# Performance work log

Measured on AMD Instinct MI355X. Metric: run time of the kernel, lower is better.

## Reference

```python
import jax, jax.numpy as jnp
import numpy as np

N = 50000
E = 1600000
IN_DIM = 256
HID = 64
OUT = 16
NEG_SLOPE = 0.01


def setup_inputs() -> dict:
    key = jax.random.key(0)
    ks = jax.random.split(key, 6)
    local_features = jax.random.normal(ks[0], (N, IN_DIM), dtype=jnp.float32)
    edge_index = jax.random.randint(ks[1], (2, E), 0, N, dtype=jnp.int32)
    W0 = jax.random.normal(ks[2], (IN_DIM, HID), dtype=jnp.float32) * 0.05
    a0 = jax.random.normal(ks[3], (2 * HID, 1), dtype=jnp.float32) * 0.05
    W1 = jax.random.normal(ks[4], (HID, OUT), dtype=jnp.float32) * 0.05
    a1 = jax.random.normal(ks[5], (2 * OUT, 1), dtype=jnp.float32) * 0.05
    return {"local_features": local_features, "edge_index": edge_index,
            "W0": W0, "a0": a0, "W1": W1, "a1": a1}


def _segment_softmax(scores, seg, num_segments):
    # softmax over edges sharing the same row (destination) id
    smax = jax.ops.segment_max(scores, seg, num_segments=num_segments)
    ex = jnp.exp(scores - smax[seg])
    ssum = jax.ops.segment_sum(ex, seg, num_segments=num_segments)
    return ex / ssum[seg]


def _gat_layer(H, row, col, W, a, apply_elu):
    d = W.shape[1]
    Hw = H @ W                                   # [N, d]
    # score_e = leaky_relu([Hw[row] || Hw[col]] @ a) = leaky_relu(pr[row] + pc[col])
    pr = Hw @ a[:d, 0]                           # [N]
    pc = Hw @ a[d:, 0]                           # [N]
    s = pr[row] + pc[col]                        # [E]
    s = jnp.where(s >= 0, s, NEG_SLOPE * s)      # leaky_relu
    att = _segment_softmax(s, row, Hw.shape[0])  # per-row sparse softmax (dim=1)
    # out[row] = sum_e att_e * Hw[col_e]
    out = jax.ops.segment_sum(att[:, None] * Hw[col], row, num_segments=Hw.shape[0])
    if apply_elu:
        out = jnp.where(out > 0, out, jnp.expm1(out))  # elu
    return out


def reference(local_features, edge_index, W0, a0, W1, a1):
    row = edge_index[0]
    col = edge_index[1]
    H = _gat_layer(local_features, row, col, W0, a0, apply_elu=True)
    H = _gat_layer(H, row, col, W1, a1, apply_elu=False)
    return jax.nn.log_softmax(H, axis=1)
```

## Files before the change

kernel.cpp:

```cpp
#include <hip/hip_runtime.h>
#include <hip/hip_bf16.h>
#include <math.h>

#define NN 50000
#define NE 1600000
#define BSH 9
#define BCK 98
#define BCAP 20480
#define GEMM_BLKS 98

typedef __attribute__((ext_vector_type(8))) short bf16x8;
typedef __attribute__((ext_vector_type(4))) float f32x4;
typedef __attribute__((ext_vector_type(2))) float f32x2;

__device__ __forceinline__ short f2bf(float f) {
    return (short)((__float_as_uint(f) + 0x8000u) >> 16);
}
__device__ __forceinline__ float lo16(unsigned u) { return __uint_as_float(u << 16); }
__device__ __forceinline__ float hi16(unsigned u) { return __uint_as_float(u & 0xffff0000u); }
__device__ __forceinline__ unsigned enc_f(float f) {
    unsigned u = __float_as_uint(f);
    return (u & 0x80000000u) ? ~u : (u | 0x80000000u);
}
__device__ __forceinline__ float dec_f(unsigned e) {
    return (e & 0x80000000u) ? __uint_as_float(e & 0x7FFFFFFFu)
                             : __uint_as_float(~e);
}

__global__ void setup_kernel(int* __restrict__ gcursor, unsigned* __restrict__ maxes,
                             unsigned* __restrict__ max1s,
                             const float* __restrict__ W, ushort* __restrict__ WTg) {
    int b = blockIdx.x;
    int t = threadIdx.x;
    if (b == 0) {
        if (t < BCK) gcursor[t] = t * BCAP;
        if (t < 2) maxes[t] = 0u;
        for (int i = t; i < 512; i += 256) max1s[i] = 0u;
    } else {
        int i = (b - 1) * 256 + t;
        int n = i >> 8, k = i & 255;
        WTg[n * 264 + k] = (ushort)f2bf(W[k * 64 + n]);
    }
}

__global__ void __launch_bounds__(1024) gbinA_kernel(
        const float* __restrict__ X,
        const ushort* __restrict__ WTg,
        const float* __restrict__ a,
        __hip_bfloat16* __restrict__ Hwb,
        float* __restrict__ pr,
        float* __restrict__ pc,
        unsigned* __restrict__ max0,
        const int* __restrict__ row, const int* __restrict__ col,
        int* __restrict__ gcursor, unsigned* __restrict__ staging) {
    __shared__ union SH {
        struct {
            unsigned lds_stage[8192];
            unsigned lds_addr[8192];
            int lds_cnt[128];
            int lds_off[128];
            int wg_goff[128];
            int wtot[2];
        } a;
        struct {
            ushort Wt[64 * 264];
            unsigned bmax;
        } g;
    } sh;
    int tid = threadIdx.x;

    if (blockIdx.x < GEMM_BLKS) {
        if (tid == 0) sh.g.bmax = 0u;
        {
            const uint* src = (const uint*)WTg;
            uint* dst = (uint*)sh.g.Wt;
            for (int i = tid; i < 64 * 132; i += 1024) dst[i] = src[i];
        }
        __syncthreads();
        int g256 = tid >> 8, t256 = tid & 255;
        int lane = t256 & 63, wid = t256 >> 6;
        int c = lane & 15, quad = lane >> 4;
        const ushort* wtp[4];
#pragma unroll
        for (int g = 0; g < 4; ++g) wtp[g] = &sh.g.Wt[(g * 16 + c) * 264 + quad * 8];
        float aA[4], aB[4];
#pragma unroll
        for (int g = 0; g < 4; ++g) { aA[g] = a[g * 16 + c]; aB[g] = a[64 + g * 16 + c]; }

        int row0 = blockIdx.x * 512 + g256 * 128 + wid * 16;
        float qmax = -1e30f;

#pragma unroll
        for (int tt = 0; tt < 2; ++tt) {
            int rt = row0 + tt * 64;
            int arow = rt + c; if (arow >= NN) arow = NN - 1;
            const float* xbase = X + (size_t)arow * 256 + quad * 8;
            f32x4 acc[4];
#pragma unroll
            for (int g = 0; g < 4; ++g) acc[g] = (f32x4){0.f, 0.f, 0.f, 0.f};

#pragma unroll
            for (int k0 = 0; k0 < 256; k0 += 32) {
                float4 xa = *(const float4*)(xbase + k0);
                float4 xb = *(const float4*)(xbase + k0 + 4);
                bf16x8 af;
                af[0] = f2bf(xa.x); af[1] = f2bf(xa.y); af[2] = f2bf(xa.z); af[3] = f2bf(xa.w);
                af[4] = f2bf(xb.x); af[5] = f2bf(xb.y); af[6] = f2bf(xb.z); af[7] = f2bf(xb.w);
#pragma unroll
                for (int g = 0; g < 4; ++g) {
                    bf16x8 bg = *(const bf16x8*)(wtp[g] + k0);
                    acc[g] = __builtin_amdgcn_mfma_f32_16x16x32_bf16(af, bg, acc[g], 0, 0, 0);
                }
            }

#pragma unroll
            for (int r = 0; r < 4; ++r) {
                int rr = rt + quad * 4 + r;
                float v0 = acc[0][r], v1 = acc[1][r], v2 = acc[2][r], v3 = acc[3][r];
                if (rr < NN) {
                    __hip_bfloat16* hp = Hwb + (size_t)rr * 64 + c;
                    hp[0]  = __float2bfloat16(v0);
                    hp[16] = __float2bfloat16(v1);
                    hp[32] = __float2bfloat16(v2);
                    hp[48] = __float2bfloat16(v3);
                }
                float pv = v0 * aA[0] + v1 * aA[1] + v2 * aA[2] + v3 * aA[3];
                float qv = v0 * aB[0] + v1 * aB[1] + v2 * aB[2] + v3 * aB[3];
#pragma unroll
                for (int off = 8; off; off >>= 1) {
                    pv += __shfl_xor(pv, off);
                    qv += __shfl_xor(qv, off);
                }
                if (c == 0 && rr < NN) { pr[rr] = pv; pc[rr] = qv; }
                if (rr < NN) qmax = fmaxf(qmax, qv);
            }
        }
        qmax = fmaxf(qmax, __shfl_xor(qmax, 16));
        qmax = fmaxf(qmax, __shfl_xor(qmax, 32));
        if (lane == 0) atomicMax(&sh.g.bmax, enc_f(qmax));
        __syncthreads();
        if (tid == 0) atomicMax(max0, sh.g.bmax);
        return;
    }

    int t = tid;
    int lane = t & 63;
    int w = t >> 6;
    int nbin = gridDim.x - GEMM_BLKS;

    for (int cb = (blockIdx.x - GEMM_BLKS) * 8192; cb < NE; cb += nbin * 8192) {
        int cnt_edges = NE - cb; if (cnt_edges > 8192) cnt_edges = 8192;
        if (t < 128) sh.a.lds_cnt[t] = 0;
        __syncthreads();
        int myb[8]; int mylo[8]; unsigned mypk[8];
        int e0 = cb + t * 8;
        if (t * 8 + 7 < cnt_edges) {
            int4 r0 = *(const int4*)(row + e0);
            int4 r1 = *(const int4*)(row + e0 + 4);
            int4 c0 = *(const int4*)(col + e0);
            int4 c1 = *(const int4*)(col + e0 + 4);
            int rr[8] = {r0.x, r0.y, r0.z, r0.w, r1.x, r1.y, r1.z, r1.w};
            int cc[8] = {c0.x, c0.y, c0.z, c0.w, c1.x, c1.y, c1.z, c1.w};
            #pragma unroll
            for (int i = 0; i < 8; ++i) {
                int b = rr[i] >> BSH;
                myb[i] = b;
                mypk[i] = ((unsigned)(rr[i] & 511) << 16) | (unsigned)cc[i];
                mylo[i] = atomicAdd(&sh.a.lds_cnt[b], 1);
            }
        } else {
            #pragma unroll
            for (int i = 0; i < 8; ++i) {
                int idx = t * 8 + i;
                myb[i] = -1;
                if (idx < cnt_edges) {
                    int e = cb + idx;
                    int r = row[e], c = col[e];
                    myb[i] = r >> BSH;
                    mypk[i] = ((unsigned)(r & 511) << 16) | (unsigned)c;
                    mylo[i] = atomicAdd(&sh.a.lds_cnt[myb[i]], 1);
                }
            }
        }
        __syncthreads();
        int v = (t < 128) ? sh.a.lds_cnt[t] : 0;
        int x = v;
        #pragma unroll
        for (int off = 1; off < 64; off <<= 1) {
            int y = __shfl_up(x, off);
            if (lane >= off) x += y;
        }
        if (t < 128 && lane == 63) sh.a.wtot[w] = x;
        __syncthreads();
        int add = (w == 1) ? sh.a.wtot[0] : 0;
        if (t < 128) sh.a.lds_off[t] = x - v + add;
        if (t < BCK) {
            int cc2 = sh.a.lds_cnt[t];
            sh.a.wg_goff[t] = cc2 ? atomicAdd(&gcursor[t], cc2) : 0;
        }
        __syncthreads();
        #pragma unroll
        for (int i = 0; i < 8; ++i) if (myb[i] >= 0) {
            int p = sh.a.lds_off[myb[i]] + mylo[i];
            sh.a.lds_stage[p] = mypk[i];
            sh.a.lds_addr[p] = (unsigned)(sh.a.wg_goff[myb[i]] + mylo[i]);
        }
        __syncthreads();
        for (int i = t; i < cnt_edges; i += 1024)
            staging[sh.a.lds_addr[i]] = sh.a.lds_stage[i];
        __syncthreads();
    }
}

__global__ void __launch_bounds__(1024) binB_kernel(
        const int* __restrict__ gcursor,
        const unsigned* __restrict__ staging,
        int* __restrict__ rowptr,
        ushort* __restrict__ colperm) {
    __shared__ int bsc[128];
    __shared__ int bw[2];
    __shared__ int cur[512];
    __shared__ int wls8[8];
    __shared__ ushort lds_col[BCAP];
    int b = blockIdx.x;
    int t = threadIdx.x;
    int lane = t & 63;
    int w = t >> 6;

    if (t < 128) {
        int v = 0;
        if (t < BCK) {
            v = gcursor[t] - t * BCAP;
            if (v > BCAP) v = BCAP;
        }
        int x = v;
        #pragma unroll
        for (int off = 1; off < 64; off <<= 1) {
            int y = __shfl_up(x, off);
            if (lane >= off) x += y;
        }
        if (lane == 63) bw[w] = x;
        bsc[t] = x - v;
    }
    __syncthreads();
    int gbase = bsc[b] + ((b >= 64) ? bw[0] : 0);
    int cnt = gcursor[b] - b * BCAP;
    if (cnt > BCAP) cnt = BCAP;
    if (b == 0 && t == 0) rowptr[NN] = bw[0] + bw[1];
    int rbase = b << BSH;
    int nrows = NN - rbase; if (nrows > 512) nrows = 512;
    const unsigned* sb = staging + (size_t)b * BCAP;

    unsigned ev[20];
    #pragma unroll
    for (int j = 0; j < 5; ++j) {
        int i0 = t * 4 + j * 4096;
        uint4 val = {0u, 0u, 0u, 0u};
        if (i0 + 3 < cnt) {
            val = *(const uint4*)(sb + i0);
        } else {
            if (i0 + 0 < cnt) val.x = sb[i0 + 0];
            if (i0 + 1 < cnt) val.y = sb[i0 + 1];
            if (i0 + 2 < cnt) val.z = sb[i0 + 2];
            if (i0 + 3 < cnt) val.w = sb[i0 + 3];
        }
        ev[j * 4 + 0] = val.x; ev[j * 4 + 1] = val.y;
        ev[j * 4 + 2] = val.z; ev[j * 4 + 3] = val.w;
    }

    if (t < 512) cur[t] = 0;
    __syncthreads();
    #pragma unroll
    for (int j = 0; j < 5; ++j) {
        #pragma unroll
        for (int l = 0; l < 4; ++l) {
            int idx = t * 4 + j * 4096 + l;
            if (idx < cnt) atomicAdd(&cur[ev[j * 4 + l] >> 16], 1);
        }
    }
    __syncthreads();
    int v = 0, x = 0;
    if (t < 512) {
        v = cur[t];
        x = v;
        #pragma unroll
        for (int off = 1; off < 64; off <<= 1) {
            int y = __shfl_up(x, off);
            if (lane >= off) x += y;
        }
        if (lane == 63) wls8[w] = x;
    }
    __syncthreads();
    if (t < 8) {
        int s = wls8[t];
        #pragma unroll
        for (int off = 1; off < 8; off <<= 1) {
            int y = __shfl_up(s, off, 8);
            if ((t & 7) >= off) s += y;
        }
        wls8[t] = s;
    }
    __syncthreads();
    int excl = 0;
    if (t < 512) {
        excl = x - v + ((w > 0) ? wls8[w - 1] : 0);
        if (t < nrows) rowptr[rbase + t] = gbase + excl;
    }
    __syncthreads();
    if (t < 512) cur[t] = excl;
    __syncthreads();
    #pragma unroll
    for (int j = 0; j < 5; ++j) {
        #pragma unroll
        for (int l = 0; l < 4; ++l) {
            int idx = t * 4 + j * 4096 + l;
            if (idx < cnt) {
                unsigned e = ev[j * 4 + l];
                int pos = atomicAdd(&cur[e >> 16], 1);
                lds_col[pos] = (ushort)(e & 0xFFFFu);
            }
        }
    }
    __syncthreads();
    for (int i = t; i < cnt; i += 1024)
        colperm[gbase + i] = lds_col[i];
}

__global__ void __launch_bounds__(256) node0_kernel(
        const int* __restrict__ rowptr,
        const ushort* __restrict__ colperm,
        const float* __restrict__ pr,
        const float* __restrict__ pc,
        const unsigned* __restrict__ pcmax,
        const ushort* __restrict__ Hwb,
        const float* __restrict__ W1,
        const float* __restrict__ a1,
        __hip_bfloat16* __restrict__ Hw1b,
        float* __restrict__ pr1,
        float* __restrict__ pc1,
        unsigned* __restrict__ max1s) {
    __shared__ float W1s[64 * 17];
    __shared__ float a1s[32];
    __shared__ float hbuf[4][64];
    __shared__ unsigned long long wcbuf[4][64];
    __shared__ unsigned bmax1;
    int t = threadIdx.x;
    if (t == 0) bmax1 = 0u;
    for (int i = t; i < 64 * 16; i += 256)
        W1s[(i >> 4) * 17 + (i & 15)] = W1[i];
    if (t < 32) a1s[t] = a1[t];
    __syncthreads();

    int lane = t & 63;
    int wid = t >> 6;
    int node = blockIdx.x * 4 + wid;
    int k = lane & 15, q = lane >> 4;
    int start = rowptr[node], end = rowptr[node + 1];
    float pri = pr[node];
    float m = pri + dec_f(*pcmax);
    m = (m >= 0.f) ? m : 0.01f * m;

    float wsum = 0.f;
    f32x2 accA = {0.f, 0.f}, accB = {0.f, 0.f};
    for (int base = start; base < end; base += 64) {
        int n = end - base; if (n > 64) n = 64;
        float wv = 0.f; unsigned cv = 0;
        if (lane < n) {
            cv = (unsigned)colperm[base + lane];
            float s = pri + pc[cv];
            s = (s >= 0.f) ? s : 0.01f * s;
            wv = __expf(s - m);
        }
        wsum += wv;
        wcbuf[wid][lane] = ((unsigned long long)cv << 32) |
                           (unsigned long long)__float_as_uint(wv);
        int iters = (n + 3) >> 2;
        #pragma unroll 4
        for (int jj = 0; jj < iters; ++jj) {
            unsigned long long wc = wcbuf[wid][jj * 4 + q];
            float wj = __uint_as_float((unsigned)wc);
            int cj = (int)(wc >> 32);
            uint2 hv = *(const uint2*)(Hwb + (size_t)cj * 64 + k * 4);
            f32x2 wj2 = {wj, wj};
            f32x2 h01 = {lo16(hv.x), hi16(hv.x)};
            f32x2 h23 = {lo16(hv.y), hi16(hv.y)};
            accA += wj2 * h01;
            accB += wj2 * h23;
        }
    }
#pragma unroll
    for (int off = 32; off; off >>= 1) wsum += __shfl_xor(wsum, off);
    float acc0 = accA.x, acc1 = accA.y, acc2 = accB.x, acc3 = accB.y;
    acc0 += __shfl_xor(acc0, 16); acc0 += __shfl_xor(acc0, 32);
    acc1 += __shfl_xor(acc1, 16); acc1 += __shfl_xor(acc1, 32);
    acc2 += __shfl_xor(acc2, 16); acc2 += __shfl_xor(acc2, 32);
    acc3 += __shfl_xor(acc3, 16); acc3 += __shfl_xor(acc3, 32);

    float inv = (wsum > 0.f) ? 1.f / wsum : 0.f;
    float h0 = acc0 * inv; h0 = (h0 > 0.f) ? h0 : (__expf(h0) - 1.f);
    float h1 = acc1 * inv; h1 = (h1 > 0.f) ? h1 : (__expf(h1) - 1.f);
    float h2 = acc2 * inv; h2 = (h2 > 0.f) ? h2 : (__expf(h2) - 1.f);
    float h3 = acc3 * inv; h3 = (h3 > 0.f) ? h3 : (__expf(h3) - 1.f);
    if (q == 0) {
        float4 hh = {h0, h1, h2, h3};
        *(float4*)&hbuf[wid][k * 4] = hh;
    }
    int j = lane & 15, p = lane >> 4;
    const float* hbp = hbuf[wid];
    float vj = 0.f;
#pragma unroll
    for (int i = 0; i < 16; ++i) {
        int kk = p * 16 + i;
        vj = fmaf(hbp[kk], W1s[kk * 17 + j], vj);
    }
    vj += __shfl_xor(vj, 16);
    vj += __shfl_xor(vj, 32);
    if (p == 0) Hw1b[(size_t)node * 16 + j] = __float2bfloat16(vj);
    float pv = vj * a1s[j];
    float qv = vj * a1s[16 + j];
#pragma unroll
    for (int off = 8; off; off >>= 1) {
        pv += __shfl_xor(pv, off);
        qv += __shfl_xor(qv, off);
    }
    if (lane == 0) {
        pr1[node] = pv; pc1[node] = qv;
        atomicMax(&bmax1, enc_f(qv));
    }
    __syncthreads();
    if (t == 0) atomicMax(&max1s[(blockIdx.x & 31) * 16], bmax1);
}

__global__ void __launch_bounds__(256) node1_kernel(
        const int* __restrict__ rowptr,
        const ushort* __restrict__ colperm,
        const float* __restrict__ pr,
        const float* __restrict__ pc,
        const unsigned* __restrict__ max1s,
        const ushort* __restrict__ Hwb,
        float* __restrict__ out) {
    __shared__ unsigned long long wcbuf[4][64];
    __shared__ unsigned gmx;
    int t = threadIdx.x;
    if (t < 32) {
        unsigned v = max1s[t * 16];
        #pragma unroll
        for (int off = 16; off; off >>= 1) {
            unsigned o = (unsigned)__shfl_xor((int)v, off, 32);
            v = (v > o) ? v : o;
        }
        if (t == 0) gmx = v;
    }
    __syncthreads();
    int lane = t & 63;
    int wid = t >> 6;
    int node = blockIdx.x * 4 + wid;
    int k = lane & 3, q = lane >> 2;
    int start = rowptr[node], end = rowptr[node + 1];
    float pri = pr[node];
    float m = pri + dec_f(gmx);
    m = (m >= 0.f) ? m : 0.01f * m;

    float wsum = 0.f;
    f32x2 accA = {0.f, 0.f}, accB = {0.f, 0.f};
    for (int base = start; base < end; base += 64) {
        int n = end - base; if (n > 64) n = 64;
        float wv = 0.f; unsigned cv = 0;
        if (lane < n) {
            cv = (unsigned)colperm[base + lane];
            float s = pri + pc[cv];
            s = (s >= 0.f) ? s : 0.01f * s;
            wv = __expf(s - m);
        }
        wsum += wv;
        wcbuf[wid][lane] = ((unsigned long long)cv << 32) |
                           (unsigned long long)__float_as_uint(wv);
        int iters = (n + 15) >> 4;
        #pragma unroll 4
        for (int jj = 0; jj < iters; ++jj) {
            unsigned long long wc = wcbuf[wid][jj * 16 + q];
            float wj = __uint_as_float((unsigned)wc);
            int cj = (int)(wc >> 32);
            uint2 hv = *(const uint2*)(Hwb + (size_t)cj * 16 + k * 4);
            f32x2 wj2 = {wj, wj};
            accA += wj2 * (f32x2){lo16(hv.x), hi16(hv.x)};
            accB += wj2 * (f32x2){lo16(hv.y), hi16(hv.y)};
        }
    }
#pragma unroll
    for (int off = 32; off; off >>= 1) wsum += __shfl_xor(wsum, off);
    float ac[4] = {accA.x, accA.y, accB.x, accB.y};
#pragma unroll
    for (int j4 = 0; j4 < 4; ++j4) {
        ac[j4] += __shfl_xor(ac[j4], 4);
        ac[j4] += __shfl_xor(ac[j4], 8);
        ac[j4] += __shfl_xor(ac[j4], 16);
        ac[j4] += __shfl_xor(ac[j4], 32);
    }
    float inv = (wsum > 0.f) ? 1.f / wsum : 0.f;
    float v0 = ac[0] * inv, v1 = ac[1] * inv;
    float v2 = ac[2] * inv, v3 = ac[3] * inv;
    float mm = fmaxf(fmaxf(v0, v1), fmaxf(v2, v3));
    mm = fmaxf(mm, __shfl_xor(mm, 1, 4));
    mm = fmaxf(mm, __shfl_xor(mm, 2, 4));
    float ssx = __expf(v0 - mm) + __expf(v1 - mm) + __expf(v2 - mm) + __expf(v3 - mm);
    ssx += __shfl_xor(ssx, 1, 4);
    ssx += __shfl_xor(ssx, 2, 4);
    float lse = mm + __logf(ssx);
    if (q == 0) {
        float4 o = {v0 - lse, v1 - lse, v2 - lse, v3 - lse};
        *(float4*)(out + (size_t)node * 16 + k * 4) = o;
    }
}

extern "C" void kernel_launch(void* const* d_in, const int* in_sizes, int n_in,
                              void* d_out, int out_size, void* d_ws, size_t ws_size,
                              hipStream_t stream) {
    const float* X  = (const float*)d_in[0];
    const int*   ei = (const int*)d_in[1];
    const float* W0 = (const float*)d_in[2];
    const float* a0 = (const float*)d_in[3];
    const float* W1 = (const float*)d_in[4];
    const float* a1 = (const float*)d_in[5];
    float* out = (float*)d_out;

    const int* row = ei;
    const int* col = ei + NE;

    char* wsb = (char*)d_ws;
    size_t off = 0;
    auto alloc = [&](size_t bytes) {
        void* p = wsb + off;
        off += (bytes + 15) & ~(size_t)15;
        return p;
    };
    unsigned* maxes = (unsigned*)alloc(16);
    unsigned* max1s = (unsigned*)alloc(512 * 4);
    int* rowptr     = (int*)alloc((NN + 2) * 4);
    int* gcursor    = (int*)alloc(128 * 4);
    unsigned* staging = (unsigned*)alloc((size_t)BCK * BCAP * 4);
    ushort* colperm = (ushort*)alloc((size_t)NE * 2);
    ushort* WTg     = (ushort*)alloc((size_t)64 * 264 * 2);
    __hip_bfloat16* Hw0b = (__hip_bfloat16*)alloc((size_t)NN * 64 * 2);
    float* pr0      = (float*)alloc(NN * 4);
    float* pc0      = (float*)alloc(NN * 4);
    __hip_bfloat16* Hw1b = (__hip_bfloat16*)alloc((size_t)NN * 16 * 2);
    float* pr1      = (float*)alloc(NN * 4);
    float* pc1      = (float*)alloc(NN * 4);

    setup_kernel<<<65, 256, 0, stream>>>(gcursor, maxes, max1s, W0, WTg);
    gbinA_kernel<<<GEMM_BLKS + 196, 1024, 0, stream>>>(X, WTg, a0, Hw0b, pr0, pc0,
                                                       &maxes[0], row, col,
                                                       gcursor, staging);
    binB_kernel<<<BCK, 1024, 0, stream>>>(gcursor, staging, rowptr, colperm);

    node0_kernel<<<NN / 4, 256, 0, stream>>>(rowptr, colperm, pr0, pc0,
                                             &maxes[0], (const ushort*)Hw0b,
                                             W1, a1, Hw1b, pr1, pc1, max1s);

    node1_kernel<<<NN / 4, 256, 0, stream>>>(rowptr, colperm, pr1, pc1,
                                             max1s, (const ushort*)Hw1b, out);
}
```

Before: 211.4 us.

## Use finer row buckets for CSR binning and drop the setup kernel

Destination-row buckets shrink from 512 rows to 128 rows (391 buckets), so the binB kernel runs 391 smaller blocks instead of 98 large ones. Each of those blocks holds fewer registers and less LDS and uses a two-wave scan. The setup kernel is removed: counters are zeroed with hipMemsetAsync, and each GEMM block transposes and converts W0 to bf16 into LDS on its own. This cuts a launch and improves parallelism in binB, at the cost of larger per-chunk scans and more global cursor atomics in binA, plus redundant W0 conversion in every GEMM block.

New measurement: 206.0 us, median of 2. -2.5%, faster.

```diff
diff --git a/kernel.cpp b/kernel.cpp
--- a/kernel.cpp
+++ b/kernel.cpp
@@ -4,9 +4,9 @@
 
 #define NN 50000
 #define NE 1600000
-#define BSH 9
-#define BCK 98
-#define BCAP 20480
+#define BSH 7
+#define BCK 391
+#define BCAP 5120
 #define GEMM_BLKS 98
 
 typedef __attribute__((ext_vector_type(8))) short bf16x8;
@@ -27,25 +27,9 @@
                              : __uint_as_float(~e);
 }
 
-__global__ void setup_kernel(int* __restrict__ gcursor, unsigned* __restrict__ maxes,
-                             unsigned* __restrict__ max1s,
-                             const float* __restrict__ W, ushort* __restrict__ WTg) {
-    int b = blockIdx.x;
-    int t = threadIdx.x;
-    if (b == 0) {
-        if (t < BCK) gcursor[t] = t * BCAP;
-        if (t < 2) maxes[t] = 0u;
-        for (int i = t; i < 512; i += 256) max1s[i] = 0u;
-    } else {
-        int i = (b - 1) * 256 + t;
-        int n = i >> 8, k = i & 255;
-        WTg[n * 264 + k] = (ushort)f2bf(W[k * 64 + n]);
-    }
-}
-
 __global__ void __launch_bounds__(1024) gbinA_kernel(
         const float* __restrict__ X,
-        const ushort* __restrict__ WTg,
+        const float* __restrict__ W0,
         const float* __restrict__ a,
         __hip_bfloat16* __restrict__ Hwb,
         float* __restrict__ pr,
@@ -57,10 +41,10 @@
         struct {
             unsigned lds_stage[8192];
             unsigned lds_addr[8192];
-            int lds_cnt[128];
-            int lds_off[128];
-            int wg_goff[128];
-            int wtot[2];
+            int lds_cnt[512];
+            int lds_off[512];
+            int wg_goff[512];
+            int wtot[8];
         } a;
         struct {
             ushort Wt[64 * 264];
@@ -71,11 +55,8 @@
 
     if (blockIdx.x < GEMM_BLKS) {
         if (tid == 0) sh.g.bmax = 0u;
-        {
-            const uint* src = (const uint*)WTg;
-            uint* dst = (uint*)sh.g.Wt;
-            for (int i = tid; i < 64 * 132; i += 1024) dst[i] = src[i];
-        }
+        for (int i = tid; i < 16384; i += 1024)
+            sh.g.Wt[(i & 63) * 264 + (i >> 6)] = (ushort)f2bf(W0[i]);
         __syncthreads();
         int g256 = tid >> 8, t256 = tid & 255;
         int lane = t256 & 63, wid = t256 >> 6;
@@ -150,7 +131,7 @@
 
     for (int cb = (blockIdx.x - GEMM_BLKS) * 8192; cb < NE; cb += nbin * 8192) {
         int cnt_edges = NE - cb; if (cnt_edges > 8192) cnt_edges = 8192;
-        if (t < 128) sh.a.lds_cnt[t] = 0;
+        if (t < 512) sh.a.lds_cnt[t] = 0;
         __syncthreads();
         int myb[8]; int mylo[8]; unsigned mypk[8];
         int e0 = cb + t * 8;
@@ -165,7 +146,7 @@
             for (int i = 0; i < 8; ++i) {
                 int b = rr[i] >> BSH;
                 myb[i] = b;
-                mypk[i] = ((unsigned)(rr[i] & 511) << 16) | (unsigned)cc[i];
+                mypk[i] = ((unsigned)(rr[i] & 127) << 16) | (unsigned)cc[i];
                 mylo[i] = atomicAdd(&sh.a.lds_cnt[b], 1);
             }
         } else {
@@ -177,26 +158,38 @@
                     int e = cb + idx;
                     int r = row[e], c = col[e];
                     myb[i] = r >> BSH;
-                    mypk[i] = ((unsigned)(r & 511) << 16) | (unsigned)c;
+                    mypk[i] = ((unsigned)(r & 127) << 16) | (unsigned)c;
                     mylo[i] = atomicAdd(&sh.a.lds_cnt[myb[i]], 1);
                 }
             }
         }
         __syncthreads();
-        int v = (t < 128) ? sh.a.lds_cnt[t] : 0;
+        int v = (t < 512) ? sh.a.lds_cnt[t] : 0;
         int x = v;
         #pragma unroll
         for (int off = 1; off < 64; off <<= 1) {
             int y = __shfl_up(x, off);
             if (lane >= off) x += y;
         }
-        if (t < 128 && lane == 63) sh.a.wtot[w] = x;
-        __syncthreads();
-        int add = (w == 1) ? sh.a.wtot[0] : 0;
-        if (t < 128) sh.a.lds_off[t] = x - v + add;
+        if (t < 512 && lane == 63) sh.a.wtot[w] = x;
+        __syncthreads();
+        if (t < 8) {
+            int s = sh.a.wtot[t];
+            #pragma unroll
+            for (int off = 1; off < 8; off <<= 1) {
+                int y = __shfl_up(s, off, 8);
+                if ((t & 7) >= off) s += y;
+            }
+            sh.a.wtot[t] = s;
+        }
+        __syncthreads();
+        if (t < 512) {
+            int add = (w > 0) ? sh.a.wtot[w - 1] : 0;
+            sh.a.lds_off[t] = x - v + add;
+        }
         if (t < BCK) {
             int cc2 = sh.a.lds_cnt[t];
-            sh.a.wg_goff[t] = cc2 ? atomicAdd(&gcursor[t], cc2) : 0;
+            sh.a.wg_goff[t] = t * BCAP + (cc2 ? atomicAdd(&gcursor[t], cc2) : 0);
         }
         __syncthreads();
         #pragma unroll
@@ -217,20 +210,20 @@
         const unsigned* __restrict__ staging,
         int* __restrict__ rowptr,
         ushort* __restrict__ colperm) {
-    __shared__ int bsc[128];
-    __shared__ int bw[2];
-    __shared__ int cur[512];
-    __shared__ int wls8[8];
+    __shared__ int bsc[512];
+    __shared__ int bw[8];
+    __shared__ int cur[128];
+    __shared__ int wls2[2];
     __shared__ ushort lds_col[BCAP];
     int b = blockIdx.x;
     int t = threadIdx.x;
     int lane = t & 63;
     int w = t >> 6;
 
-    if (t < 128) {
+    if (t < 512) {
         int v = 0;
         if (t < BCK) {
-            v = gcursor[t] - t * BCAP;
+            v = gcursor[t];
             if (v > BCAP) v = BCAP;
         }
         int x = v;
@@ -243,17 +236,27 @@
         bsc[t] = x - v;
     }
     __syncthreads();
-    int gbase = bsc[b] + ((b >= 64) ? bw[0] : 0);
-    int cnt = gcursor[b] - b * BCAP;
+    if (t < 8) {
+        int s = bw[t];
+        #pragma unroll
+        for (int off = 1; off < 8; off <<= 1) {
+            int y = __shfl_up(s, off, 8);
+            if ((t & 7) >= off) s += y;
+        }
+        bw[t] = s;
+    }
+    __syncthreads();
+    int gbase = bsc[b] + ((b >= 64) ? bw[(b >> 6) - 1] : 0);
+    int cnt = gcursor[b];
     if (cnt > BCAP) cnt = BCAP;
-    if (b == 0 && t == 0) rowptr[NN] = bw[0] + bw[1];
+    if (b == 0 && t == 0) rowptr[NN] = bw[7];
     int rbase = b << BSH;
-    int nrows = NN - rbase; if (nrows > 512) nrows = 512;
+    int nrows = NN - rbase; if (nrows > 128) nrows = 128;
     const unsigned* sb = staging + (size_t)b * BCAP;
 
-    unsigned ev[20];
+    unsigned ev[8];
     #pragma unroll
-    for (int j = 0; j < 5; ++j) {
+    for (int j = 0; j < 2; ++j) {
         int i0 = t * 4 + j * 4096;
         uint4 val = {0u, 0u, 0u, 0u};
         if (i0 + 3 < cnt) {
@@ -268,10 +271,10 @@
         ev[j * 4 + 2] = val.z; ev[j * 4 + 3] = val.w;
     }
 
-    if (t < 512) cur[t] = 0;
+    if (t < 128) cur[t] = 0;
     __syncthreads();
     #pragma unroll
-    for (int j = 0; j < 5; ++j) {
+    for (int j = 0; j < 2; ++j) {
         #pragma unroll
         for (int l = 0; l < 4; ++l) {
             int idx = t * 4 + j * 4096 + l;
@@ -280,7 +283,7 @@
     }
     __syncthreads();
     int v = 0, x = 0;
-    if (t < 512) {
+    if (t < 128) {
         v = cur[t];
         x = v;
         #pragma unroll
@@ -288,29 +291,19 @@
             int y = __shfl_up(x, off);
             if (lane >= off) x += y;
         }
-        if (lane == 63) wls8[w] = x;
-    }
-    __syncthreads();
-    if (t < 8) {
-        int s = wls8[t];
-        #pragma unroll
-        for (int off = 1; off < 8; off <<= 1) {
-            int y = __shfl_up(s, off, 8);
-            if ((t & 7) >= off) s += y;
-        }
-        wls8[t] = s;
+        if (lane == 63) wls2[w] = x;
     }
     __syncthreads();
     int excl = 0;
-    if (t < 512) {
-        excl = x - v + ((w > 0) ? wls8[w - 1] : 0);
+    if (t < 128) {
+        excl = x - v + ((w == 1) ? wls2[0] : 0);
         if (t < nrows) rowptr[rbase + t] = gbase + excl;
     }
     __syncthreads();
-    if (t < 512) cur[t] = excl;
+    if (t < 128) cur[t] = excl;
     __syncthreads();
     #pragma unroll
-    for (int j = 0; j < 5; ++j) {
+    for (int j = 0; j < 2; ++j) {
         #pragma unroll
         for (int l = 0; l < 4; ++l) {
             int idx = t * 4 + j * 4096 + l;
@@ -536,11 +529,11 @@
     };
     unsigned* maxes = (unsigned*)alloc(16);
     unsigned* max1s = (unsigned*)alloc(512 * 4);
+    int* gcursor    = (int*)alloc(512 * 4);
+    size_t zinit = off;
     int* rowptr     = (int*)alloc((NN + 2) * 4);
-    int* gcursor    = (int*)alloc(128 * 4);
     unsigned* staging = (unsigned*)alloc((size_t)BCK * BCAP * 4);
     ushort* colperm = (ushort*)alloc((size_t)NE * 2);
-    ushort* WTg     = (ushort*)alloc((size_t)64 * 264 * 2);
     __hip_bfloat16* Hw0b = (__hip_bfloat16*)alloc((size_t)NN * 64 * 2);
     float* pr0      = (float*)alloc(NN * 4);
     float* pc0      = (float*)alloc(NN * 4);
@@ -548,8 +541,9 @@
     float* pr1      = (float*)alloc(NN * 4);
     float* pc1      = (float*)alloc(NN * 4);
 
-    setup_kernel<<<65, 256, 0, stream>>>(gcursor, maxes, max1s, W0, WTg);
-    gbinA_kernel<<<GEMM_BLKS + 196, 1024, 0, stream>>>(X, WTg, a0, Hw0b, pr0, pc0,
+    hipMemsetAsync(wsb, 0, zinit, stream);
+
+    gbinA_kernel<<<GEMM_BLKS + 196, 1024, 0, stream>>>(X, W0, a0, Hw0b, pr0, pc0,
                                                        &maxes[0], row, col,
                                                        gcursor, staging);
     binB_kernel<<<BCK, 1024, 0, stream>>>(gcursor, staging, rowptr, colperm);
```
